# Kernel optimization log

Measured on AMD Instinct MI355X. Metric: run time of the kernel, lower is better.

The kernel has to match this reference:

```python
import jax, jax.numpy as jnp
import numpy as np

B, T, L, A, O = 16, 32, 64, 64, 16
EL, EA, EO = 128, 128, 128
FL, FA, FO, C = 256, 256, 256, 768


def setup_inputs() -> dict:
    key = jax.random.key(0)
    ks = jax.random.split(key, 16)
    s = 0.02
    return {
        "lab_feats": jax.random.normal(ks[0], (B, T, L, FL), jnp.float32),
        "abn_feats": jax.random.normal(ks[1], (B, T, A, FA), jnp.float32),
        "lab_concept_emb": jax.random.normal(ks[2], (L, C), jnp.float32),
        "abn_concept_emb": jax.random.normal(ks[3], (A, C), jnp.float32),
        "lab_rel_emb": jax.random.normal(ks[4], (EL, C), jnp.float32),
        "abn_rel_emb": jax.random.normal(ks[5], (EA, C), jnp.float32),
        "W_lab": jax.random.normal(ks[6], (FL + C, FL), jnp.float32) * s,
        "b_lab": jnp.zeros((FL,), jnp.float32),
        "W_abn": jax.random.normal(ks[7], (FA + C, FA), jnp.float32) * s,
        "b_abn": jnp.zeros((FA,), jnp.float32),
        "W_org": jax.random.normal(ks[8], (FL, FO), jnp.float32) * s,
        "b_org": jnp.zeros((FO,), jnp.float32),
        "D": jax.random.normal(ks[9], (C, FL), jnp.float32) * s,
        "W_o2a": jax.random.normal(ks[10], (FO, FA), jnp.float32) * s,
        "b_o2a": jnp.zeros((FA,), jnp.float32),
        "time_mask": jnp.ones((B, T), dtype=bool),
        "lab_idx": jax.random.randint(ks[11], (EL,), 0, L),
        "lab_org_idx": jax.random.randint(ks[12], (EL,), 0, O),
        "abn_idx": jax.random.randint(ks[13], (EA,), 0, A),
        "abn_org_idx": jax.random.randint(ks[14], (EA,), 0, O),
        "o2a_abn_idx": jax.random.randint(ks[15], (EO,), 0, A),
        "o2a_org_idx": jax.random.randint(jax.random.fold_in(key, 99), (EO,), 0, O),
        "num_organs": O,
    }


def _scatter_mean(attended, org_idx, num_organs, time_mask):
    # attended: (B,T,E,F); emulate legacy per-edge accumulate: cnt[o] = deg(o)*w(b,t)
    onehot = (org_idx[:, None] == jnp.arange(num_organs)[None, :]).astype(attended.dtype)  # (E,O)
    sum_o = jnp.einsum('btef,eo->btof', attended, onehot)
    deg = onehot.sum(0)                                    # (O,)
    w = time_mask.astype(attended.dtype)                   # (B,T)
    cnt = w[:, :, None] * deg[None, None, :]               # (B,T,O)
    mean_o = sum_o / jnp.maximum(cnt, 1e-9)[..., None]
    return mean_o, cnt > 0


def reference(lab_feats, abn_feats, lab_concept_emb, abn_concept_emb,
              lab_rel_emb, abn_rel_emb, W_lab, b_lab, W_abn, b_abn,
              W_org, b_org, D, W_o2a, b_o2a,
              time_mask, lab_idx, lab_org_idx, abn_idx, abn_org_idx,
              o2a_abn_idx, o2a_org_idx, num_organs):
    Fl = lab_feats.shape[-1]
    Fa = abn_feats.shape[-1]
    A_ = abn_feats.shape[2]

    # --- lab -> organ: gather, concat(feat, concept+relation), W_lab (split to avoid concat) ---
    x = lab_feats[:, :, lab_idx, :]                        # (B,T,El,Fl)
    c = lab_concept_emb[lab_idx] + lab_rel_emb             # (El,C)
    h = jnp.tanh(jnp.einsum('btef,fg->bteg', x, W_lab[:Fl]) + c @ W_lab[Fl:] + b_lab)
    attended = h + lab_rel_emb @ D                         # relation-projection D
    mean_lab, mask_lab = _scatter_mean(attended, lab_org_idx, num_organs, time_mask)

    # --- abn -> organ ---
    xa = abn_feats[:, :, abn_idx, :]
    ca = abn_concept_emb[abn_idx] + abn_rel_emb
    ha = jnp.tanh(jnp.einsum('btef,fg->bteg', xa, W_abn[:Fa]) + ca @ W_abn[Fa:] + b_abn)
    mean_abn, mask_abn = _scatter_mean(ha, abn_org_idx, num_organs, time_mask)

    # --- organ states ---
    organ_states = jnp.tanh(jnp.einsum('btof,fg->btog', mean_lab + mean_abn, W_org) + b_org)
    organ_states = organ_states * (mask_lab | mask_abn)[..., None].astype(organ_states.dtype)

    # --- organ -> abnormality message passing (mean over incident organs) ---
    msg = jnp.einsum('btog,gf->btof', organ_states, W_o2a) + b_o2a   # (B,T,O,Fa)
    gathered = msg[:, :, o2a_org_idx, :]                   # (B,T,Eo,Fa)
    onehot = (o2a_abn_idx[:, None] == jnp.arange(A_)[None, :]).astype(msg.dtype)  # (Eo,A)
    agg = jnp.einsum('btef,ea->btaf', gathered, onehot)
    deg = jnp.maximum(onehot.sum(0), 1.0)                  # (A,)
    abn_out = abn_feats + agg / deg[None, None, :, None]
    return abn_out
```

## Files before the change

### kernel.cpp

```cpp
#include <hip/hip_runtime.h>
#include <math.h>

#define NBT 512
#define NF  256
#define NC  768
#define NROW 64
#define NORG 16
#define NE  128
#define SLD 260
#define SY  264

#define WS_SW_LAB1 0
#define WS_SW_ABN1 131072
#define WS_SW_LAB2 262144
#define WS_SW_D    655360
#define WS_SW_ABN2 1048576
#define WS_SW_ORG  1441792
#define WS_SW_O2A  1572864
#define WS_SUMREL  1703936
#define WS_LAB_CB  1753088
#define WS_ABN_CB  1884160
#define WS_ADDSUM  2015232
#define WS_WCNT    2031616
#define WS_INVL    2035712
#define WS_INVA    2035776
#define WS_MASK    2035840
#define WS_SRTL    2035904
#define WS_SRTA    2036544
#define WS_RAWL    2097152
#define WS_RAWA    10485760
#define WS_NEED    18874368

typedef __attribute__((ext_vector_type(8)))  short bf16x8;
typedef __attribute__((ext_vector_type(16))) float f32x16;
typedef __attribute__((ext_vector_type(4)))  float f32x4;

__device__ __forceinline__ short f2bf(float f) {
    union { float f; unsigned u; } v; v.f = f;
    unsigned r = v.u + 0x7FFF + ((v.u >> 16) & 1);
    return (short)(r >> 16);
}
__device__ __forceinline__ float bf2f(short s) {
    return __uint_as_float(((unsigned)(unsigned short)s) << 16);
}
__device__ __forceinline__ float tanh_fast(float x) {
    float xc = fminf(fmaxf(x, -15.f), 15.f);
    float e = __expf(2.f * xc);
    return 1.f - 2.f * __builtin_amdgcn_rcpf(e + 1.f);
}
__device__ __forceinline__ f32x16 mfma32(bf16x8 a, bf16x8 b, f32x16 c) {
    return __builtin_amdgcn_mfma_f32_32x32x16_bf16(a, b, c, 0, 0, 0);
}
__device__ __forceinline__ f32x4 mfma16(bf16x8 a, bf16x8 b, f32x4 c) {
    return __builtin_amdgcn_mfma_f32_16x16x32_bf16(a, b, c, 0, 0, 0);
}
__device__ __forceinline__ bf16x8 pack_a16(const float* __restrict__ p) {
    float4 x0 = *(const float4*)p;
    float4 x1 = *(const float4*)(p + 4);
    union { bf16x8 v; unsigned u[4]; } r;
    r.u[0] = __builtin_amdgcn_perm(__float_as_uint(x0.y), __float_as_uint(x0.x), 0x07060302);
    r.u[1] = __builtin_amdgcn_perm(__float_as_uint(x0.w), __float_as_uint(x0.z), 0x07060302);
    r.u[2] = __builtin_amdgcn_perm(__float_as_uint(x1.y), __float_as_uint(x1.x), 0x07060302);
    r.u[3] = __builtin_amdgcn_perm(__float_as_uint(x1.w), __float_as_uint(x1.z), 0x07060302);
    return r.v;
}

__device__ __forceinline__ void swz32(const float* __restrict__ src, short* __restrict__ dst, int s) {
    const int l = s & 63, rest = s >> 6;
    const int nt = rest & 7, k16 = rest >> 3;
    const int n = nt * 32 + (l & 31);
    const int kb = k16 * 16 + ((l >> 5) & 1) * 8;
    bf16x8 v;
    #pragma unroll
    for (int j = 0; j < 8; ++j) v[j] = f2bf(src[(kb + j) * NF + n]);
    *(bf16x8*)(dst + s * 8) = v;
}
__device__ __forceinline__ void swz16(const float* __restrict__ src, short* __restrict__ dst, int s) {
    const int l = s & 63, rest = s >> 6;
    const int nt = rest & 15, k32 = rest >> 4;
    const int n = nt * 16 + (l & 15);
    const int kb = k32 * 32 + ((l >> 4) & 3) * 8;
    bf16x8 v;
    #pragma unroll
    for (int j = 0; j < 8; ++j) v[j] = f2bf(src[(kb + j) * NF + n]);
    *(bf16x8*)(dst + s * 8) = v;
}

__global__ __launch_bounds__(256) void pk_pre(
    const float* __restrict__ W_lab, const float* __restrict__ W_abn,
    const float* __restrict__ D, const float* __restrict__ W_org,
    const float* __restrict__ W_o2a, const float* __restrict__ lab_rel,
    const int* __restrict__ lab_idx, const int* __restrict__ lab_org_idx,
    const int* __restrict__ abn_idx, const int* __restrict__ abn_org_idx,
    const int* __restrict__ o2a_abn_idx, const int* __restrict__ o2a_org_idx,
    char* __restrict__ ws) {
    const int bid = blockIdx.x;
    if (bid < 416) {
        const int gid = bid * 256 + threadIdx.x;
        if      (gid <  8192) swz32(W_lab,           (short*)(ws + WS_SW_LAB1), gid);
        else if (gid < 16384) swz32(W_abn,           (short*)(ws + WS_SW_ABN1), gid - 8192);
        else if (gid < 40960) swz32(W_lab + NF * NF, (short*)(ws + WS_SW_LAB2), gid - 16384);
        else if (gid < 65536) swz32(D,               (short*)(ws + WS_SW_D),    gid - 40960);
        else if (gid < 90112) swz32(W_abn + NF * NF, (short*)(ws + WS_SW_ABN2), gid - 65536);
        else if (gid < 98304) swz16(W_org,           (short*)(ws + WS_SW_ORG),  gid - 90112);
        else                  swz16(W_o2a,           (short*)(ws + WS_SW_O2A),  gid - 98304);
    } else if (bid == 416) {
        __shared__ int cL[NORG], cA[NORG], cC[NROW * NORG];
        __shared__ int goL[NORG + 1], goA[NORG + 1], curL[NORG], curA[NORG];
        const int t = threadIdx.x;
        for (int i = t; i < NROW * NORG; i += 256) cC[i] = 0;
        if (t < NORG) { cL[t] = 0; cA[t] = 0; }
        __syncthreads();
        if (t < NE) {
            atomicAdd(&cL[lab_org_idx[t]], 1);
            atomicAdd(&cA[abn_org_idx[t]], 1);
            atomicAdd(&cC[o2a_abn_idx[t] * NORG + o2a_org_idx[t]], 1);
        }
        __syncthreads();
        if (t == 0) { int s = 0; for (int o = 0; o < NORG; ++o) { goL[o] = s; s += cL[o]; } goL[NORG] = s; }
        if (t == 1) { int s = 0; for (int o = 0; o < NORG; ++o) { goA[o] = s; s += cA[o]; } goA[NORG] = s; }
        __syncthreads();
        if (t < NORG) { curL[t] = goL[t]; curA[t] = goA[t]; }
        __syncthreads();
        if (t < NE) {
            const int ol = lab_org_idx[t], oa = abn_org_idx[t];
            int p = atomicAdd(&curL[ol], 1);
            ((int*)(ws + WS_SRTL))[p] = (lab_idx[t] << 24) | (ol << 16) | t;
            int q = atomicAdd(&curA[oa], 1);
            ((int*)(ws + WS_SRTA))[q] = (abn_idx[t] << 24) | (oa << 16) | t;
        }
        if (t < NORG) {
            ((float*)(ws + WS_INVL))[t] = cL[t] ? 1.f / (float)cL[t] : 0.f;
            ((float*)(ws + WS_INVA))[t] = cA[t] ? 1.f / (float)cA[t] : 0.f;
            ((float*)(ws + WS_MASK))[t] = (cL[t] || cA[t]) ? 1.f : 0.f;
        }
        if (t < NROW) {
            int dega = 0;
            for (int o = 0; o < NORG; ++o) dega += cC[t * NORG + o];
            float inv = 1.f / (float)(dega > 1 ? dega : 1);
            for (int o = 0; o < NORG; ++o)
                ((float*)(ws + WS_WCNT))[t * NORG + o] = (float)cC[t * NORG + o] * inv;
        }
    } else {
        const int b2 = bid - 417;
        const int o = b2 / 3, kth = b2 % 3;
        const int k = kth * 256 + threadIdx.x;
        float s = 0.f;
        #pragma unroll 16
        for (int e = 0; e < NE; ++e) {
            const float v = lab_rel[e * NC + k];
            s += (lab_org_idx[e] == o) ? v : 0.f;
        }
        ((float*)(ws + WS_SUMREL))[o * NC + k] = s;
    }
}

__global__ __launch_bounds__(256) void pk_bias2(
    const float* __restrict__ lab_con, const float* __restrict__ abn_con,
    const float* __restrict__ lab_rel, const float* __restrict__ abn_rel,
    const float* __restrict__ b_lab, const float* __restrict__ b_abn,
    const int* __restrict__ lab_idx, const int* __restrict__ abn_idx,
    char* __restrict__ ws) {
    __shared__ __align__(16) float sP[4 * 1024];
    const int tid = threadIdx.x, l = tid & 63, w = tid >> 6;
    const int bid = blockIdx.x;
    const int kbase = w * 192;

    f32x16 acc;
    #pragma unroll
    for (int r = 0; r < 16; ++r) acc[r] = 0.f;

    if (bid < 64) {
        const int side = bid >> 5;
        const int b2 = bid & 31;
        const int mq = b2 >> 3, nb = b2 & 7;
        const int em = mq * 32;
        const short* Bsw = (const short*)(ws + (side ? WS_SW_ABN2 : WS_SW_LAB2));
        const float* con = side ? abn_con : lab_con;
        const float* rel = side ? abn_rel : lab_rel;
        const int*   idx = side ? abn_idx : lab_idx;

        const int e  = em + (l & 31);
        const int kk = ((l >> 5) & 1) * 8;
        const float* cp = con + idx[e] * NC;
        const float* rp = rel + e * NC;
        #pragma unroll 4
        for (int k16 = 0; k16 < 12; ++k16) {
            const int k = kbase + k16 * 16 + kk;
            float4 c0 = *(const float4*)(cp + k);
            float4 c1 = *(const float4*)(cp + k + 4);
            float4 r0 = *(const float4*)(rp + k);
            float4 r1 = *(const float4*)(rp + k + 4);
            float v[8] = {c0.x + r0.x, c0.y + r0.y, c0.z + r0.z, c0.w + r0.w,
                          c1.x + r1.x, c1.y + r1.y, c1.z + r1.z, c1.w + r1.w};
            bf16x8 af;
            #pragma unroll
            for (int j = 0; j < 8; ++j) af[j] = f2bf(v[j]);
            bf16x8 bv = *(const bf16x8*)(Bsw + (((w * 12 + k16) * 8 + nb) * 64 + l) * 8);
            acc = mfma32(af, bv, acc);
        }
        #pragma unroll
        for (int r = 0; r < 16; ++r) sP[w * 1024 + r * 64 + l] = acc[r];
        __syncthreads();
        float* outp = (float*)(ws + (side ? WS_ABN_CB : WS_LAB_CB));
        const float* bias = side ? b_abn : b_lab;
        #pragma unroll
        for (int q = 0; q < 4; ++q) {
            const int idx2 = q * 256 + tid;
            float v = sP[idx2] + sP[1024 + idx2] + sP[2048 + idx2] + sP[3072 + idx2];
            const int reg = idx2 >> 6, ll = idx2 & 63;
            const int er = (reg & 3) + 8 * (reg >> 2) + 4 * (ll >> 5);
            const int col = nb * 32 + (ll & 31);
            outp[(em + er) * NF + col] = v + bias[col];
        }
    } else {
        const int nb = bid - 64;
        const short* Bsw = (const short*)(ws + WS_SW_D);
        const float* sr = (const float*)(ws + WS_SUMREL);

        const int row = l & 31;
        const int kk = ((l >> 5) & 1) * 8;
        const float* cp = sr + row * NC;
        #pragma unroll 4
        for (int k16 = 0; k16 < 12; ++k16) {
            const int k = kbase + k16 * 16 + kk;
            bf16x8 af;
            if (row < NORG) {
                af = pack_a16(cp + k);
            } else {
                #pragma unroll
                for (int j = 0; j < 8; ++j) af[j] = 0;
            }
            bf16x8 bv = *(const bf16x8*)(Bsw + (((w * 12 + k16) * 8 + nb) * 64 + l) * 8);
            acc = mfma32(af, bv, acc);
        }
        #pragma unroll
        for (int r = 0; r < 16; ++r) sP[w * 1024 + r * 64 + l] = acc[r];
        __syncthreads();
        float* outp = (float*)(ws + WS_ADDSUM);
        #pragma unroll
        for (int q = 0; q < 4; ++q) {
            const int idx2 = q * 256 + tid;
            float v = sP[idx2] + sP[1024 + idx2] + sP[2048 + idx2] + sP[3072 + idx2];
            const int reg = idx2 >> 6, ll = idx2 & 63;
            const int er = (reg & 3) + 8 * (reg >> 2) + 4 * (ll >> 5);
            const int col = nb * 32 + (ll & 31);
            if (er < NORG) outp[er * NF + col] = v;
        }
    }
}

__device__ __forceinline__ void stage_A(const float* __restrict__ X, short* __restrict__ sA, int tid) {
    #pragma unroll
    for (int ss = 0; ss < 8; ++ss) {
        const int s = tid + 256 * ss;
        const int k16 = s >> 7, rt = (s >> 6) & 1, l = s & 63;
        const int row = rt * 32 + (l & 31);
        const int kb = k16 * 16 + ((l >> 5) & 1) * 8;
        *(bf16x8*)(sA + s * 8) = pack_a16(X + row * NF + kb);
    }
}

template <int POST>
__device__ __forceinline__ void gemm_small(
    const float* __restrict__ sIn, const short* __restrict__ Bsw,
    const float* __restrict__ bias, const float* __restrict__ mask,
    float* __restrict__ sOut, int tid) {
    const int l = tid & 63, w = tid >> 6;
    f32x4 acc[4];
    #pragma unroll
    for (int i = 0; i < 4; ++i) { acc[i][0] = 0.f; acc[i][1] = 0.f; acc[i][2] = 0.f; acc[i][3] = 0.f; }
    #pragma unroll 2
    for (int k32 = 0; k32 < 8; ++k32) {
        const float* ap = sIn + (l & 15) * SLD + k32 * 32 + ((l >> 4) & 3) * 8;
        bf16x8 af = pack_a16(ap);
        #pragma unroll
        for (int nt = 0; nt < 4; ++nt) {
            bf16x8 bfv = *(const bf16x8*)(Bsw + ((k32 * 16 + w * 4 + nt) * 64 + l) * 8);
            acc[nt] = mfma16(af, bfv, acc[nt]);
        }
    }
    #pragma unroll
    for (int nt = 0; nt < 4; ++nt) {
        const int col = w * 64 + nt * 16 + (l & 15);
        const float b = bias[col];
        #pragma unroll
        for (int reg = 0; reg < 4; ++reg) {
            const int row = ((l >> 4) & 3) * 4 + reg;
            float v = acc[nt][reg] + b;
            if (POST == 0) v = tanh_fast(v) * mask[row];
            sOut[row * SLD + col] = v;
        }
    }
}

__global__ __launch_bounds__(256, 4) void kg_side(
    const float* __restrict__ lab_feats, const float* __restrict__ abn_feats,
    char* __restrict__ ws) {
    __shared__ __align__(16) short sY[NROW * SY];
    __shared__ int sE[NE];

    const int tid = threadIdx.x;
    const int side = blockIdx.x >> 9;
    const int bt = blockIdx.x & 511;

    if (tid < NE) sE[tid] = ((const int*)(ws + (side ? WS_SRTA : WS_SRTL)))[tid];

    const float* X   = (side ? abn_feats : lab_feats) + bt * (NROW * NF);
    const short* Bsw = (const short*)(ws + (side ? WS_SW_ABN1 : WS_SW_LAB1));
    const float* cb  = (const float*)(ws + (side ? WS_ABN_CB : WS_LAB_CB));
    float* rawo = (float*)(ws + (side ? WS_RAWA : WS_RAWL)) + bt * (NORG * NF);

    stage_A(X, sY, tid);
    __syncthreads();

    const int l = tid & 63, w = tid >> 6;
    f32x16 acc[2][2];
    #pragma unroll
    for (int i = 0; i < 2; ++i)
        #pragma unroll
        for (int j = 0; j < 2; ++j)
            #pragma unroll
            for (int r = 0; r < 16; ++r) acc[i][j][r] = 0.f;
    #pragma unroll 8
    for (int k16 = 0; k16 < 16; ++k16) {
        bf16x8 a0 = *(const bf16x8*)(sY + ((k16 * 2 + 0) * 64 + l) * 8);
        bf16x8 a1 = *(const bf16x8*)(sY + ((k16 * 2 + 1) * 64 + l) * 8);
        bf16x8 b0 = *(const bf16x8*)(Bsw + ((k16 * 8 + 2 * w + 0) * 64 + l) * 8);
        bf16x8 b1 = *(const bf16x8*)(Bsw + ((k16 * 8 + 2 * w + 1) * 64 + l) * 8);
        acc[0][0] = mfma32(a0, b0, acc[0][0]);
        acc[1][0] = mfma32(a1, b0, acc[1][0]);
        acc[0][1] = mfma32(a0, b1, acc[0][1]);
        acc[1][1] = mfma32(a1, b1, acc[1][1]);
    }
    __syncthreads();
    #pragma unroll
    for (int rt = 0; rt < 2; ++rt)
        #pragma unroll
        for (int nt = 0; nt < 2; ++nt) {
            const int col = w * 64 + nt * 32 + (l & 31);
            #pragma unroll
            for (int reg = 0; reg < 16; ++reg) {
                const int row = rt * 32 + (reg & 3) + 8 * (reg >> 2) + 4 * (l >> 5);
                sY[row * SY + col] = f2bf(acc[rt][nt][reg]);
            }
        }
    __syncthreads();

    const int t = tid;
    float racc = 0.f;
    int curo = (__builtin_amdgcn_readfirstlane(sE[0]) >> 16) & 255;
    for (int i0 = 0; i0 < NE; i0 += 8) {
        int   pk8[8];
        float cb8[8], y8[8];
        #pragma unroll
        for (int j = 0; j < 8; ++j) {
            const int pk = __builtin_amdgcn_readfirstlane(sE[i0 + j]);
            pk8[j] = pk;
            cb8[j] = cb[(pk & 0xffff) * NF + t];
            y8[j]  = bf2f(sY[(pk >> 24) * SY + t]);
        }
        #pragma unroll
        for (int j = 0; j < 8; ++j) {
            const int o = (pk8[j] >> 16) & 255;
            if (o != curo) {
                rawo[curo * NF + t] = racc;
                racc = 0.f; curo = o;
            }
            racc += tanh_fast(y8[j] + cb8[j]);
        }
    }
    rawo[curo * NF + t] = racc;
}

__global__ __launch_bounds__(256, 4) void kg_back(
    const float* __restrict__ abn_feats, const float* __restrict__ b_org,
    const float* __restrict__ b_o2a, const char* __restrict__ ws,
    float* __restrict__ out) {
    __shared__ __align__(16) float sIn[NORG * SLD];
    __shared__ __align__(16) float sSt[NORG * SLD];
    __shared__ float sWc[NROW * NORG];
    __shared__ float sInvL[NORG], sInvA[NORG], sMsk[NORG];

    const int tid = threadIdx.x;
    const int bt = blockIdx.x;

    if      (tid < NORG)     sInvL[tid]          = ((const float*)(ws + WS_INVL))[tid];
    else if (tid < 2 * NORG) sInvA[tid - NORG]   = ((const float*)(ws + WS_INVA))[tid - NORG];
    else if (tid < 3 * NORG) sMsk[tid - 2 * NORG] = ((const float*)(ws + WS_MASK))[tid - 2 * NORG];
    #pragma unroll
    for (int i = tid; i < NROW * NORG; i += 256)
        sWc[i] = ((const float*)(ws + WS_WCNT))[i];

    const float* rawL = (const float*)(ws + WS_RAWL) + bt * (NORG * NF);
    const float* rawA = (const float*)(ws + WS_RAWA) + bt * (NORG * NF);
    const float* addR = (const float*)(ws + WS_ADDSUM);
    __syncthreads();

    const int g = tid;
    #pragma unroll
    for (int o = 0; o < NORG; ++o) {
        const float il = sInvL[o], ia = sInvA[o];
        const float vl = (il > 0.f) ? (rawL[o * NF + g] + addR[o * NF + g]) * il : 0.f;
        const float va = (ia > 0.f) ? rawA[o * NF + g] * ia : 0.f;
        sIn[o * SLD + g] = vl + va;
    }
    __syncthreads();

    gemm_small<0>(sIn, (const short*)(ws + WS_SW_ORG), b_org, sMsk, sSt, tid);
    __syncthreads();
    gemm_small<1>(sSt, (const short*)(ws + WS_SW_O2A), b_o2a, nullptr, sIn, tid);
    __syncthreads();

    float mr[NORG];
    #pragma unroll
    for (int o = 0; o < NORG; ++o) mr[o] = sIn[o * SLD + g];
    const float* src = abn_feats + bt * (NROW * NF);
    float* dst = out + bt * (NROW * NF);
    #pragma unroll 4
    for (int a = 0; a < NROW; ++a) {
        float s = src[a * NF + g];
        #pragma unroll
        for (int o = 0; o < NORG; ++o) s += sWc[a * NORG + o] * mr[o];
        dst[a * NF + g] = s;
    }
}

template <bool LAB>
__device__ __forceinline__ void side_pass(
    const float* __restrict__ X, const short* __restrict__ Bsw,
    const float* __restrict__ cb, const float* __restrict__ addR,
    const float* __restrict__ sInv, const int* __restrict__ sE,
    short* __restrict__ sA, float* __restrict__ sAcc, int tid) {
    __syncthreads();
    stage_A(X, sA, tid);
    __syncthreads();
    const int l = tid & 63, w = tid >> 6;
    f32x16 acc[2][2];
    #pragma unroll
    for (int i = 0; i < 2; ++i)
        #pragma unroll
        for (int j = 0; j < 2; ++j)
            #pragma unroll
            for (int r = 0; r < 16; ++r) acc[i][j][r] = 0.f;
    #pragma unroll 8
    for (int k16 = 0; k16 < 16; ++k16) {
        bf16x8 a0 = *(const bf16x8*)(sA + ((k16 * 2 + 0) * 64 + l) * 8);
        bf16x8 a1 = *(const bf16x8*)(sA + ((k16 * 2 + 1) * 64 + l) * 8);
        bf16x8 b0 = *(const bf16x8*)(Bsw + ((k16 * 8 + 2 * w + 0) * 64 + l) * 8);
        bf16x8 b1 = *(const bf16x8*)(Bsw + ((k16 * 8 + 2 * w + 1) * 64 + l) * 8);
        acc[0][0] = mfma32(a0, b0, acc[0][0]);
        acc[1][0] = mfma32(a1, b0, acc[1][0]);
        acc[0][1] = mfma32(a0, b1, acc[0][1]);
        acc[1][1] = mfma32(a1, b1, acc[1][1]);
    }
    __syncthreads();
    short* sYs = sA;
    #pragma unroll
    for (int rt = 0; rt < 2; ++rt)
        #pragma unroll
        for (int nt = 0; nt < 2; ++nt) {
            const int col = w * 64 + nt * 32 + (l & 31);
            #pragma unroll
            for (int reg = 0; reg < 16; ++reg) {
                const int row = rt * 32 + (reg & 3) + 8 * (reg >> 2) + 4 * (l >> 5);
                sYs[row * SY + col] = f2bf(acc[rt][nt][reg]);
            }
        }
    __syncthreads();
    const int t = tid;
    if (LAB) {
        #pragma unroll
        for (int o = 0; o < NORG; ++o)
            sAcc[o * SLD + t] = addR[o * NF + t] * sInv[o];
    }
    float racc = 0.f;
    int curo = (sE[0] >> 16) & 255;
    #pragma unroll 4
    for (int i = 0; i < NE; ++i) {
        const int pk = sE[i];
        const int o = (pk >> 16) & 255;
        if (o != curo) {
            sAcc[curo * SLD + t] += racc * sInv[curo];
            racc = 0.f; curo = o;
        }
        const float yv = bf2f(sYs[(pk >> 24) * SY + t]);
        racc += tanh_fast(yv + cb[(pk & 0xffff) * NF + t]);
    }
    sAcc[curo * SLD + t] += racc * sInv[curo];
}

__global__ __launch_bounds__(256, 2) void kg_main(
    const float* __restrict__ lab_feats, const float* __restrict__ abn_feats,
    const float* __restrict__ b_org, const float* __restrict__ b_o2a,
    const char* __restrict__ ws, float* __restrict__ out) {
    __shared__ __align__(16) short sY[NROW * SY];
    __shared__ __align__(16) float sAcc[NORG * SLD];
    __shared__ __align__(16) float sSt [NORG * SLD];
    __shared__ int   sEL[NE], sEA[NE];
    __shared__ float sInvL[NORG], sInvA[NORG], sMsk[NORG];

    const int tid = threadIdx.x;
    const int bt = blockIdx.x;

    if (tid < NE) {
        sEL[tid] = ((const int*)(ws + WS_SRTL))[tid];
        sEA[tid] = ((const int*)(ws + WS_SRTA))[tid];
    } else {
        const int u = tid - NE;
        if      (u < 16) sInvL[u]      = ((const float*)(ws + WS_INVL))[u];
        else if (u < 32) sInvA[u - 16] = ((const float*)(ws + WS_INVA))[u - 16];
        else if (u < 48) sMsk[u - 32]  = ((const float*)(ws + WS_MASK))[u - 32];
    }

    const float* Xl = lab_feats + bt * (NROW * NF);
    const float* Xa = abn_feats + bt * (NROW * NF);
    side_pass<true >(Xl, (const short*)(ws + WS_SW_LAB1),
                     (const float*)(ws + WS_LAB_CB), (const float*)(ws + WS_ADDSUM),
                     sInvL, sEL, sY, sAcc, tid);
    side_pass<false>(Xa, (const short*)(ws + WS_SW_ABN1),
                     (const float*)(ws + WS_ABN_CB), nullptr,
                     sInvA, sEA, sY, sAcc, tid);
    __syncthreads();

    gemm_small<0>(sAcc, (const short*)(ws + WS_SW_ORG), b_org, sMsk, sSt, tid);
    __syncthreads();
    float* sMsg = sAcc;
    gemm_small<1>(sSt, (const short*)(ws + WS_SW_O2A), b_o2a, nullptr, sMsg, tid);
    __syncthreads();

    {
        const int g = tid;
        float mr[NORG];
        #pragma unroll
        for (int o = 0; o < NORG; ++o) mr[o] = sMsg[o * SLD + g];
        const float* src = abn_feats + bt * (NROW * NF);
        float* dst = out + bt * (NROW * NF);
        const float* wc = (const float*)(ws + WS_WCNT);
        #pragma unroll 4
        for (int a = 0; a < NROW; ++a) {
            float s = src[a * NF + g];
            #pragma unroll
            for (int o = 0; o < NORG; ++o) s += wc[a * NORG + o] * mr[o];
            dst[a * NF + g] = s;
        }
    }
}

extern "C" void kernel_launch(void* const* d_in, const int* in_sizes, int n_in,
                              void* d_out, int out_size, void* d_ws, size_t ws_size,
                              hipStream_t stream) {
    const float* lab_feats   = (const float*)d_in[0];
    const float* abn_feats   = (const float*)d_in[1];
    const float* lab_concept = (const float*)d_in[2];
    const float* abn_concept = (const float*)d_in[3];
    const float* lab_rel     = (const float*)d_in[4];
    const float* abn_rel     = (const float*)d_in[5];
    const float* W_lab       = (const float*)d_in[6];
    const float* b_lab       = (const float*)d_in[7];
    const float* W_abn       = (const float*)d_in[8];
    const float* b_abn       = (const float*)d_in[9];
    const float* W_org       = (const float*)d_in[10];
    const float* b_org       = (const float*)d_in[11];
    const float* D           = (const float*)d_in[12];
    const float* W_o2a       = (const float*)d_in[13];
    const float* b_o2a       = (const float*)d_in[14];
    const int* lab_idx     = (const int*)d_in[16];
    const int* lab_org_idx = (const int*)d_in[17];
    const int* abn_idx     = (const int*)d_in[18];
    const int* abn_org_idx = (const int*)d_in[19];
    const int* o2a_abn_idx = (const int*)d_in[20];
    const int* o2a_org_idx = (const int*)d_in[21];
    char* ws = (char*)d_ws;
    float* out = (float*)d_out;

    pk_pre<<<465, 256, 0, stream>>>(W_lab, W_abn, D, W_org, W_o2a, lab_rel,
                                    lab_idx, lab_org_idx, abn_idx, abn_org_idx,
                                    o2a_abn_idx, o2a_org_idx, ws);
    pk_bias2<<<72, 256, 0, stream>>>(lab_concept, abn_concept, lab_rel, abn_rel,
                                     b_lab, b_abn, lab_idx, abn_idx, ws);
    if (ws_size >= (size_t)WS_NEED) {
        kg_side<<<2 * NBT, 256, 0, stream>>>(lab_feats, abn_feats, ws);
        kg_back<<<NBT, 256, 0, stream>>>(abn_feats, b_org, b_o2a, ws, out);
    } else {
        kg_main<<<NBT, 256, 0, stream>>>(lab_feats, abn_feats, b_org, b_o2a, ws, out);
    }
}
```

Before: 213.4 us.

## Fuse side and back kernels using per-timestep flags between lab and abn blocks

```diff
diff --git a/kernel.cpp b/kernel.cpp
--- a/kernel.cpp
+++ b/kernel.cpp
@@ -27,6 +27,7 @@
 #define WS_MASK    2035840
 #define WS_SRTL    2035904
 #define WS_SRTA    2036544
+#define WS_FLAGS   2037056
 #define WS_RAWL    2097152
 #define WS_RAWA    10485760
 #define WS_NEED    18874368
@@ -105,6 +106,8 @@
         else if (gid < 98304) swz16(W_org,           (short*)(ws + WS_SW_ORG),  gid - 90112);
         else                  swz16(W_o2a,           (short*)(ws + WS_SW_O2A),  gid - 98304);
     } else if (bid == 416) {
+        ((int*)(ws + WS_FLAGS))[threadIdx.x]       = 0;
+        ((int*)(ws + WS_FLAGS))[threadIdx.x + 256] = 0;
         __shared__ int cL[NORG], cA[NORG], cC[NROW * NORG];
         __shared__ int goL[NORG + 1], goA[NORG + 1], curL[NORG], curA[NORG];
         const int t = threadIdx.x;
@@ -294,17 +297,32 @@
     }
 }
 
-__global__ __launch_bounds__(256, 4) void kg_side(
+__global__ __launch_bounds__(256, 4) void kg_fused(
     const float* __restrict__ lab_feats, const float* __restrict__ abn_feats,
-    char* __restrict__ ws) {
+    const float* __restrict__ b_org, const float* __restrict__ b_o2a,
+    char* __restrict__ ws, float* __restrict__ out) {
     __shared__ __align__(16) short sY[NROW * SY];
     __shared__ int sE[NE];
+    __shared__ float sWc[NROW * NORG];
+    __shared__ float sInvL[NORG], sInvA[NORG], sMsk[NORG];
 
     const int tid = threadIdx.x;
     const int side = blockIdx.x >> 9;
     const int bt = blockIdx.x & 511;
+    int* flags = (int*)(ws + WS_FLAGS);
 
     if (tid < NE) sE[tid] = ((const int*)(ws + (side ? WS_SRTA : WS_SRTL)))[tid];
+    if (side) {
+        if (tid >= NE) {
+            const int u = tid - NE;
+            if      (u < 16) sInvL[u]      = ((const float*)(ws + WS_INVL))[u];
+            else if (u < 32) sInvA[u - 16] = ((const float*)(ws + WS_INVA))[u - 16];
+            else if (u < 48) sMsk[u - 32]  = ((const float*)(ws + WS_MASK))[u - 32];
+        }
+        #pragma unroll
+        for (int i = tid; i < NROW * NORG; i += 256)
+            sWc[i] = ((const float*)(ws + WS_WCNT))[i];
+    }
 
     const float* X   = (side ? abn_feats : lab_feats) + bt * (NROW * NF);
     const short* Bsw = (const short*)(ws + (side ? WS_SW_ABN1 : WS_SW_LAB1));
@@ -350,59 +368,57 @@
     const int t = tid;
     float racc = 0.f;
     int curo = (__builtin_amdgcn_readfirstlane(sE[0]) >> 16) & 255;
-    for (int i0 = 0; i0 < NE; i0 += 8) {
-        int   pk8[8];
-        float cb8[8], y8[8];
-        #pragma unroll
-        for (int j = 0; j < 8; ++j) {
+    for (int i0 = 0; i0 < NE; i0 += 16) {
+        int   pk16[16];
+        float cb16[16], y16[16];
+        #pragma unroll
+        for (int j = 0; j < 16; ++j) {
             const int pk = __builtin_amdgcn_readfirstlane(sE[i0 + j]);
-            pk8[j] = pk;
-            cb8[j] = cb[(pk & 0xffff) * NF + t];
-            y8[j]  = bf2f(sY[(pk >> 24) * SY + t]);
-        }
-        #pragma unroll
-        for (int j = 0; j < 8; ++j) {
-            const int o = (pk8[j] >> 16) & 255;
+            pk16[j] = pk;
+            cb16[j] = cb[(pk & 0xffff) * NF + t];
+            y16[j]  = bf2f(sY[(pk >> 24) * SY + t]);
+        }
+        #pragma unroll
+        for (int j = 0; j < 16; ++j) {
+            const int o = (pk16[j] >> 16) & 255;
             if (o != curo) {
-                rawo[curo * NF + t] = racc;
+                if (side) rawo[curo * NF + t] = racc;
+                else __hip_atomic_store(&rawo[curo * NF + t], racc,
+                                        __ATOMIC_RELAXED, __HIP_MEMORY_SCOPE_AGENT);
                 racc = 0.f; curo = o;
             }
-            racc += tanh_fast(y8[j] + cb8[j]);
-        }
-    }
-    rawo[curo * NF + t] = racc;
-}
-
-__global__ __launch_bounds__(256, 4) void kg_back(
-    const float* __restrict__ abn_feats, const float* __restrict__ b_org,
-    const float* __restrict__ b_o2a, const char* __restrict__ ws,
-    float* __restrict__ out) {
-    __shared__ __align__(16) float sIn[NORG * SLD];
-    __shared__ __align__(16) float sSt[NORG * SLD];
-    __shared__ float sWc[NROW * NORG];
-    __shared__ float sInvL[NORG], sInvA[NORG], sMsk[NORG];
-
-    const int tid = threadIdx.x;
-    const int bt = blockIdx.x;
-
-    if      (tid < NORG)     sInvL[tid]          = ((const float*)(ws + WS_INVL))[tid];
-    else if (tid < 2 * NORG) sInvA[tid - NORG]   = ((const float*)(ws + WS_INVA))[tid - NORG];
-    else if (tid < 3 * NORG) sMsk[tid - 2 * NORG] = ((const float*)(ws + WS_MASK))[tid - 2 * NORG];
-    #pragma unroll
-    for (int i = tid; i < NROW * NORG; i += 256)
-        sWc[i] = ((const float*)(ws + WS_WCNT))[i];
-
-    const float* rawL = (const float*)(ws + WS_RAWL) + bt * (NORG * NF);
-    const float* rawA = (const float*)(ws + WS_RAWA) + bt * (NORG * NF);
+            racc += tanh_fast(y16[j] + cb16[j]);
+        }
+    }
+    if (side) rawo[curo * NF + t] = racc;
+    else __hip_atomic_store(&rawo[curo * NF + t], racc,
+                            __ATOMIC_RELAXED, __HIP_MEMORY_SCOPE_AGENT);
+
+    if (!side) {
+        __syncthreads();
+        if (tid == 0)
+            __hip_atomic_store(&flags[bt], 1, __ATOMIC_RELEASE, __HIP_MEMORY_SCOPE_AGENT);
+        return;
+    }
+
+    if (tid == 0) {
+        while (__hip_atomic_load(&flags[bt], __ATOMIC_ACQUIRE, __HIP_MEMORY_SCOPE_AGENT) == 0)
+            __builtin_amdgcn_s_sleep(2);
+    }
+    __syncthreads();
+
+    float* sIn = (float*)sY;
+    float* sSt = (float*)sY + NORG * SLD;
+    float* rawL = (float*)(ws + WS_RAWL) + bt * (NORG * NF);
     const float* addR = (const float*)(ws + WS_ADDSUM);
-    __syncthreads();
-
     const int g = tid;
     #pragma unroll
     for (int o = 0; o < NORG; ++o) {
         const float il = sInvL[o], ia = sInvA[o];
-        const float vl = (il > 0.f) ? (rawL[o * NF + g] + addR[o * NF + g]) * il : 0.f;
-        const float va = (ia > 0.f) ? rawA[o * NF + g] * ia : 0.f;
+        const float rl = __hip_atomic_load(&rawL[o * NF + g],
+                                           __ATOMIC_RELAXED, __HIP_MEMORY_SCOPE_AGENT);
+        const float vl = (il > 0.f) ? (rl + addR[o * NF + g]) * il : 0.f;
+        const float va = (ia > 0.f) ? rawo[o * NF + g] * ia : 0.f;
         sIn[o * SLD + g] = vl + va;
     }
     __syncthreads();
@@ -580,8 +596,7 @@
     pk_bias2<<<72, 256, 0, stream>>>(lab_concept, abn_concept, lab_rel, abn_rel,
                                      b_lab, b_abn, lab_idx, abn_idx, ws);
     if (ws_size >= (size_t)WS_NEED) {
-        kg_side<<<2 * NBT, 256, 0, stream>>>(lab_feats, abn_feats, ws);
-        kg_back<<<NBT, 256, 0, stream>>>(abn_feats, b_org, b_o2a, ws, out);
+        kg_fused<<<2 * NBT, 256, 0, stream>>>(lab_feats, abn_feats, b_org, b_o2a, ws, out);
     } else {
         kg_main<<<NBT, 256, 0, stream>>>(lab_feats, abn_feats, b_org, b_o2a, ws, out);
     }
```

Result: slower. 218.4 us (+2.3%).

## Merge bias precompute into prep kernel and fold addsum GEMM into side kernel

Applied to the files above, without the earlier changes.

```diff
diff --git a/kernel.cpp b/kernel.cpp
--- a/kernel.cpp
+++ b/kernel.cpp
@@ -86,25 +86,27 @@
     *(bf16x8*)(dst + s * 8) = v;
 }
 
-__global__ __launch_bounds__(256) void pk_pre(
+__global__ __launch_bounds__(256) void pk_pre2(
     const float* __restrict__ W_lab, const float* __restrict__ W_abn,
     const float* __restrict__ D, const float* __restrict__ W_org,
     const float* __restrict__ W_o2a, const float* __restrict__ lab_rel,
+    const float* __restrict__ lab_con, const float* __restrict__ abn_con,
+    const float* __restrict__ abn_rel,
+    const float* __restrict__ b_lab, const float* __restrict__ b_abn,
     const int* __restrict__ lab_idx, const int* __restrict__ lab_org_idx,
     const int* __restrict__ abn_idx, const int* __restrict__ abn_org_idx,
     const int* __restrict__ o2a_abn_idx, const int* __restrict__ o2a_org_idx,
     char* __restrict__ ws) {
+    __shared__ __align__(16) float sP[4 * 1024];
     const int bid = blockIdx.x;
-    if (bid < 416) {
+    if (bid < 224) {
         const int gid = bid * 256 + threadIdx.x;
-        if      (gid <  8192) swz32(W_lab,           (short*)(ws + WS_SW_LAB1), gid);
-        else if (gid < 16384) swz32(W_abn,           (short*)(ws + WS_SW_ABN1), gid - 8192);
-        else if (gid < 40960) swz32(W_lab + NF * NF, (short*)(ws + WS_SW_LAB2), gid - 16384);
-        else if (gid < 65536) swz32(D,               (short*)(ws + WS_SW_D),    gid - 40960);
-        else if (gid < 90112) swz32(W_abn + NF * NF, (short*)(ws + WS_SW_ABN2), gid - 65536);
-        else if (gid < 98304) swz16(W_org,           (short*)(ws + WS_SW_ORG),  gid - 90112);
-        else                  swz16(W_o2a,           (short*)(ws + WS_SW_O2A),  gid - 98304);
-    } else if (bid == 416) {
+        if      (gid <  8192) swz32(W_lab, (short*)(ws + WS_SW_LAB1), gid);
+        else if (gid < 16384) swz32(W_abn, (short*)(ws + WS_SW_ABN1), gid - 8192);
+        else if (gid < 40960) swz32(D,     (short*)(ws + WS_SW_D),    gid - 16384);
+        else if (gid < 49152) swz16(W_org, (short*)(ws + WS_SW_ORG),  gid - 40960);
+        else                  swz16(W_o2a, (short*)(ws + WS_SW_O2A),  gid - 49152);
+    } else if (bid == 224) {
         __shared__ int cL[NORG], cA[NORG], cC[NROW * NORG];
         __shared__ int goL[NORG + 1], goA[NORG + 1], curL[NORG], curA[NORG];
         const int t = threadIdx.x;
@@ -141,8 +143,8 @@
             for (int o = 0; o < NORG; ++o)
                 ((float*)(ws + WS_WCNT))[t * NORG + o] = (float)cC[t * NORG + o] * inv;
         }
-    } else {
-        const int b2 = bid - 417;
+    } else if (bid < 273) {
+        const int b2 = bid - 225;
         const int o = b2 / 3, kth = b2 % 3;
         const int k = kth * 256 + threadIdx.x;
         float s = 0.f;
@@ -152,41 +154,30 @@
             s += (lab_org_idx[e] == o) ? v : 0.f;
         }
         ((float*)(ws + WS_SUMREL))[o * NC + k] = s;
-    }
-}
-
-__global__ __launch_bounds__(256) void pk_bias2(
-    const float* __restrict__ lab_con, const float* __restrict__ abn_con,
-    const float* __restrict__ lab_rel, const float* __restrict__ abn_rel,
-    const float* __restrict__ b_lab, const float* __restrict__ b_abn,
-    const int* __restrict__ lab_idx, const int* __restrict__ abn_idx,
-    char* __restrict__ ws) {
-    __shared__ __align__(16) float sP[4 * 1024];
-    const int tid = threadIdx.x, l = tid & 63, w = tid >> 6;
-    const int bid = blockIdx.x;
-    const int kbase = w * 192;
-
-    f32x16 acc;
-    #pragma unroll
-    for (int r = 0; r < 16; ++r) acc[r] = 0.f;
-
-    if (bid < 64) {
-        const int side = bid >> 5;
-        const int b2 = bid & 31;
+    } else {
+        const int tid = threadIdx.x, l = tid & 63, w = tid >> 6;
+        const int bid2 = bid - 273;
+        const int side = bid2 >> 5;
+        const int b2 = bid2 & 31;
         const int mq = b2 >> 3, nb = b2 & 7;
         const int em = mq * 32;
-        const short* Bsw = (const short*)(ws + (side ? WS_SW_ABN2 : WS_SW_LAB2));
+        const float* W2  = side ? (W_abn + NF * NF) : (W_lab + NF * NF);
         const float* con = side ? abn_con : lab_con;
         const float* rel = side ? abn_rel : lab_rel;
         const int*   idx = side ? abn_idx : lab_idx;
 
+        f32x16 acc;
+        #pragma unroll
+        for (int r = 0; r < 16; ++r) acc[r] = 0.f;
+
         const int e  = em + (l & 31);
         const int kk = ((l >> 5) & 1) * 8;
+        const int n  = nb * 32 + (l & 31);
         const float* cp = con + idx[e] * NC;
         const float* rp = rel + e * NC;
         #pragma unroll 4
         for (int k16 = 0; k16 < 12; ++k16) {
-            const int k = kbase + k16 * 16 + kk;
+            const int k = (w * 12 + k16) * 16 + kk;
             float4 c0 = *(const float4*)(cp + k);
             float4 c1 = *(const float4*)(cp + k + 4);
             float4 r0 = *(const float4*)(rp + k);
@@ -196,7 +187,10 @@
             bf16x8 af;
             #pragma unroll
             for (int j = 0; j < 8; ++j) af[j] = f2bf(v[j]);
-            bf16x8 bv = *(const bf16x8*)(Bsw + (((w * 12 + k16) * 8 + nb) * 64 + l) * 8);
+            const float* wp = W2 + k * NF + n;
+            bf16x8 bv;
+            #pragma unroll
+            for (int j = 0; j < 8; ++j) bv[j] = f2bf(wp[j * NF]);
             acc = mfma32(af, bv, acc);
         }
         #pragma unroll
@@ -213,40 +207,6 @@
             const int col = nb * 32 + (ll & 31);
             outp[(em + er) * NF + col] = v + bias[col];
         }
-    } else {
-        const int nb = bid - 64;
-        const short* Bsw = (const short*)(ws + WS_SW_D);
-        const float* sr = (const float*)(ws + WS_SUMREL);
-
-        const int row = l & 31;
-        const int kk = ((l >> 5) & 1) * 8;
-        const float* cp = sr + row * NC;
-        #pragma unroll 4
-        for (int k16 = 0; k16 < 12; ++k16) {
-            const int k = kbase + k16 * 16 + kk;
-            bf16x8 af;
-            if (row < NORG) {
-                af = pack_a16(cp + k);
-            } else {
-                #pragma unroll
-                for (int j = 0; j < 8; ++j) af[j] = 0;
-            }
-            bf16x8 bv = *(const bf16x8*)(Bsw + (((w * 12 + k16) * 8 + nb) * 64 + l) * 8);
-            acc = mfma32(af, bv, acc);
-        }
-        #pragma unroll
-        for (int r = 0; r < 16; ++r) sP[w * 1024 + r * 64 + l] = acc[r];
-        __syncthreads();
-        float* outp = (float*)(ws + WS_ADDSUM);
-        #pragma unroll
-        for (int q = 0; q < 4; ++q) {
-            const int idx2 = q * 256 + tid;
-            float v = sP[idx2] + sP[1024 + idx2] + sP[2048 + idx2] + sP[3072 + idx2];
-            const int reg = idx2 >> 6, ll = idx2 & 63;
-            const int er = (reg & 3) + 8 * (reg >> 2) + 4 * (ll >> 5);
-            const int col = nb * 32 + (ll & 31);
-            if (er < NORG) outp[er * NF + col] = v;
-        }
     }
 }
 
@@ -294,6 +254,45 @@
     }
 }
 
+__device__ __forceinline__ void addsum_body(char* __restrict__ ws, float* __restrict__ sP,
+                                            int nb, int tid) {
+    const int l = tid & 63, w = tid >> 6;
+    const short* Bsw = (const short*)(ws + WS_SW_D);
+    const float* sr = (const float*)(ws + WS_SUMREL);
+    f32x16 acc;
+    #pragma unroll
+    for (int r = 0; r < 16; ++r) acc[r] = 0.f;
+    const int row = l & 31;
+    const int kk = ((l >> 5) & 1) * 8;
+    const float* cp = sr + row * NC;
+    #pragma unroll 4
+    for (int k16 = 0; k16 < 12; ++k16) {
+        const int k = w * 192 + k16 * 16 + kk;
+        bf16x8 af;
+        if (row < NORG) {
+            af = pack_a16(cp + k);
+        } else {
+            #pragma unroll
+            for (int j = 0; j < 8; ++j) af[j] = 0;
+        }
+        bf16x8 bv = *(const bf16x8*)(Bsw + (((w * 12 + k16) * 8 + nb) * 64 + l) * 8);
+        acc = mfma32(af, bv, acc);
+    }
+    #pragma unroll
+    for (int r = 0; r < 16; ++r) sP[w * 1024 + r * 64 + l] = acc[r];
+    __syncthreads();
+    float* outp = (float*)(ws + WS_ADDSUM);
+    #pragma unroll
+    for (int q = 0; q < 4; ++q) {
+        const int idx2 = q * 256 + tid;
+        float v = sP[idx2] + sP[1024 + idx2] + sP[2048 + idx2] + sP[3072 + idx2];
+        const int reg = idx2 >> 6, ll = idx2 & 63;
+        const int er = (reg & 3) + 8 * (reg >> 2) + 4 * (ll >> 5);
+        const int col = nb * 32 + (ll & 31);
+        if (er < NORG) outp[er * NF + col] = v;
+    }
+}
+
 __global__ __launch_bounds__(256, 4) void kg_side(
     const float* __restrict__ lab_feats, const float* __restrict__ abn_feats,
     char* __restrict__ ws) {
@@ -301,8 +300,13 @@
     __shared__ int sE[NE];
 
     const int tid = threadIdx.x;
-    const int side = blockIdx.x >> 9;
-    const int bt = blockIdx.x & 511;
+    if (blockIdx.x < 8) {
+        addsum_body(ws, (float*)sY, blockIdx.x, tid);
+        return;
+    }
+    const int idx = blockIdx.x - 8;
+    const int side = idx >> 9;
+    const int bt = idx & 511;
 
     if (tid < NE) sE[tid] = ((const int*)(ws + (side ? WS_SRTA : WS_SRTL)))[tid];
 
@@ -350,24 +354,24 @@
     const int t = tid;
     float racc = 0.f;
     int curo = (__builtin_amdgcn_readfirstlane(sE[0]) >> 16) & 255;
-    for (int i0 = 0; i0 < NE; i0 += 8) {
-        int   pk8[8];
-        float cb8[8], y8[8];
-        #pragma unroll
-        for (int j = 0; j < 8; ++j) {
+    for (int i0 = 0; i0 < NE; i0 += 16) {
+        int   pk16[16];
+        float cb16[16], y16[16];
+        #pragma unroll
+        for (int j = 0; j < 16; ++j) {
             const int pk = __builtin_amdgcn_readfirstlane(sE[i0 + j]);
-            pk8[j] = pk;
-            cb8[j] = cb[(pk & 0xffff) * NF + t];
-            y8[j]  = bf2f(sY[(pk >> 24) * SY + t]);
-        }
-        #pragma unroll
-        for (int j = 0; j < 8; ++j) {
-            const int o = (pk8[j] >> 16) & 255;
+            pk16[j] = pk;
+            cb16[j] = cb[(pk & 0xffff) * NF + t];
+            y16[j]  = bf2f(sY[(pk >> 24) * SY + t]);
+        }
+        #pragma unroll
+        for (int j = 0; j < 16; ++j) {
+            const int o = (pk16[j] >> 16) & 255;
             if (o != curo) {
                 rawo[curo * NF + t] = racc;
                 racc = 0.f; curo = o;
             }
-            racc += tanh_fast(y8[j] + cb8[j]);
+            racc += tanh_fast(y16[j] + cb16[j]);
         }
     }
     rawo[curo * NF + t] = racc;
@@ -424,6 +428,11 @@
         for (int o = 0; o < NORG; ++o) s += sWc[a * NORG + o] * mr[o];
         dst[a * NF + g] = s;
     }
+}
+
+__global__ __launch_bounds__(256) void pk_addsum(char* __restrict__ ws) {
+    __shared__ __align__(16) float sP[4 * 1024];
+    addsum_body(ws, sP, blockIdx.x, threadIdx.x);
 }
 
 template <bool LAB>
@@ -574,15 +583,16 @@
     char* ws = (char*)d_ws;
     float* out = (float*)d_out;
 
-    pk_pre<<<465, 256, 0, stream>>>(W_lab, W_abn, D, W_org, W_o2a, lab_rel,
-                                    lab_idx, lab_org_idx, abn_idx, abn_org_idx,
-                                    o2a_abn_idx, o2a_org_idx, ws);
-    pk_bias2<<<72, 256, 0, stream>>>(lab_concept, abn_concept, lab_rel, abn_rel,
-                                     b_lab, b_abn, lab_idx, abn_idx, ws);
+    pk_pre2<<<337, 256, 0, stream>>>(W_lab, W_abn, D, W_org, W_o2a, lab_rel,
+                                     lab_concept, abn_concept, abn_rel,
+                                     b_lab, b_abn,
+                                     lab_idx, lab_org_idx, abn_idx, abn_org_idx,
+                                     o2a_abn_idx, o2a_org_idx, ws);
     if (ws_size >= (size_t)WS_NEED) {
-        kg_side<<<2 * NBT, 256, 0, stream>>>(lab_feats, abn_feats, ws);
+        kg_side<<<8 + 2 * NBT, 256, 0, stream>>>(lab_feats, abn_feats, ws);
         kg_back<<<NBT, 256, 0, stream>>>(abn_feats, b_org, b_o2a, ws, out);
     } else {
+        pk_addsum<<<8, 256, 0, stream>>>(ws);
         kg_main<<<NBT, 256, 0, stream>>>(lab_feats, abn_feats, b_org, b_o2a, ws, out);
     }
 }
```

After: 211.2 us. About the same (-1.1%).
